# Performance work log

Measured on AMD Instinct MI355X. Metric: run time of the kernel, lower is better.

## Reference

```python
import jax, jax.numpy as jnp
import numpy as np

B, T, N, F = 32, 64, 128, 128
U, K1, K2 = 64, 64, 32
EPS = 1e-3  # keras BatchNormalization default epsilon
SLOPE = 0.01  # LeakyReLU negative_slope


def setup_inputs() -> dict:
    key = jax.random.key(0)
    ks = jax.random.split(key, 16)
    g = lambda k, sh, s=0.05: jax.random.normal(k, sh, dtype=jnp.float32) * s
    inp = {
        "x": jax.random.normal(ks[0], (B, T, F), dtype=jnp.float32),
        "a": jax.random.uniform(ks[1], (B, N, N), dtype=jnp.float32),
        # LSTM (keras gate order i, f, c, o)
        "lstm_k": g(ks[2], (F, 4 * U)),
        "lstm_r": g(ks[3], (U, 4 * U)),
        "lstm_b": jnp.zeros((4 * U,), jnp.float32),
        # BatchNorm params (inference form: gamma, beta, moving mean, moving var)
        "bnl_g": jnp.ones((U,), jnp.float32), "bnl_b": jnp.zeros((U,), jnp.float32),
        "bnl_m": jnp.zeros((U,), jnp.float32), "bnl_v": jnp.ones((U,), jnp.float32),
        "w1": g(ks[4], (U, K1)), "b1": jnp.zeros((K1,), jnp.float32),
        "bn1_g": jnp.ones((K1,), jnp.float32), "bn1_b": jnp.zeros((K1,), jnp.float32),
        "bn1_m": jnp.zeros((K1,), jnp.float32), "bn1_v": jnp.ones((K1,), jnp.float32),
        "w2": g(ks[5], (K1, K2)), "b2": jnp.zeros((K2,), jnp.float32),
        "bn2_g": jnp.ones((K2,), jnp.float32), "bn2_b": jnp.zeros((K2,), jnp.float32),
        "bn2_m": jnp.zeros((K2,), jnp.float32), "bn2_v": jnp.ones((K2,), jnp.float32),
        "d1_w": g(ks[6], (T * N * K2, 3), 0.01), "d1_b": jnp.zeros((3,), jnp.float32),
        "d2_w": g(ks[7], (3, N)), "d2_b": jnp.zeros((N,), jnp.float32),
    }
    return inp


def _bn(x, g, b, m, v):
    return (x - m) * (g * jax.lax.rsqrt(v + EPS)) + b


def _leaky(x):
    return jnp.where(x >= 0, x, SLOPE * x)


def _lstm(x, Wk, Wr, b):
    # x: [B, T, F] -> hs: [B, T, U]
    xz = jnp.einsum('btf,fg->btg', x, Wk) + b  # precompute input projections
    u = Wr.shape[0]
    h0 = jnp.zeros((x.shape[0], u), x.dtype)
    c0 = jnp.zeros((x.shape[0], u), x.dtype)

    def step(carry, zt):
        h, c = carry
        z = zt + h @ Wr
        i, f, g_, o = jnp.split(z, 4, axis=-1)
        i = jax.nn.sigmoid(i); f = jax.nn.sigmoid(f)
        g_ = jnp.tanh(g_); o = jax.nn.sigmoid(o)
        c = f * c + i * g_
        h = o * jnp.tanh(c)
        return (h, c), h

    _, hs = jax.lax.scan(step, (h0, c0), xz.transpose(1, 0, 2))
    return hs.transpose(1, 0, 2)


def reference(x, a, lstm_k, lstm_r, lstm_b, bnl_g, bnl_b, bnl_m, bnl_v,
              w1, b1, bn1_g, bn1_b, bn1_m, bn1_v,
              w2, b2, bn2_g, bn2_b, bn2_m, bn2_v,
              d1_w, d1_b, d2_w, d2_b):
    h = _lstm(x, lstm_k, lstm_r, lstm_b)              # [B, T, U]
    h = _bn(h, bnl_g, bnl_b, bnl_m, bnl_v)            # inference BN; dropout is identity
    # tile each timestep's LSTM output over the N nodes, then GCN1
    support1 = jnp.einsum('btu,uk->btk', h, w1)       # [B, T, K1] (identical across nodes)
    sup1 = jnp.broadcast_to(support1[:, :, None, :], (h.shape[0], h.shape[1], N, w1.shape[1]))
    g1 = jnp.einsum('bij,btjk->btik', a, sup1) + b1   # adjacency matmul
    g1 = _leaky(g1)
    g1 = _bn(g1, bn1_g, bn1_b, bn1_m, bn1_v)
    # GCN2
    sup2 = jnp.einsum('btnk,km->btnm', g1, w2)
    g2 = jnp.einsum('bij,btjm->btim', a, sup2) + b2
    g2 = _leaky(g2)
    g2 = _bn(g2, bn2_g, bn2_b, bn2_m, bn2_v)          # [B, T, N, K2]
    flat = g2.reshape(g2.shape[0], -1)                # [B, T*N*K2]
    d1 = jax.nn.relu(flat @ d1_w + d1_b)              # [B, 3]
    return d1 @ d2_w + d2_b                           # [B, N]
```

## Files before the change

kernel.cpp:

```cpp
#include <hip/hip_runtime.h>

#define BB 32
#define TT 64
#define NN 128
#define FF 128
#define UU 64
#define K1 64
#define K2 32
#define G4 256
#define EPSV 1e-3f
#define SLOPE 0.01f

#define ALD 136
#define SLD 136
#define WLD 72

typedef __attribute__((ext_vector_type(8))) short short8;
typedef __attribute__((ext_vector_type(4))) float f32x4;
typedef __attribute__((ext_vector_type(2))) __fp16 half2v;

__device__ __forceinline__ float sigmoidf_(float x) {
  return __builtin_amdgcn_rcpf(1.f + __expf(-x));
}
__device__ __forceinline__ float tanhf_(float x) {
  return 1.f - 2.f * __builtin_amdgcn_rcpf(__expf(2.f * x) + 1.f);
}
__device__ __forceinline__ float leaky_(float x) { return x >= 0.f ? x : SLOPE * x; }
__device__ __forceinline__ unsigned short f2bf(float x) {
  union { float f; unsigned u; } v; v.f = x;
  unsigned r = v.u + 0x7fff + ((v.u >> 16) & 1);
  return (unsigned short)(r >> 16);
}

__global__ __launch_bounds__(256) void k_xzp(const float* __restrict__ x,
                                             const float* __restrict__ wk,
                                             const float* __restrict__ bias,
                                             const float* __restrict__ wr,
                                             const float* __restrict__ w1,
                                             float* __restrict__ xz,
                                             unsigned* __restrict__ wrp,
                                             unsigned* __restrict__ w1p) {
  int tid = threadIdx.x;
  if (blockIdx.x < 256) {
    __shared__ float xs[8][FF];
    int row0 = blockIdx.x * 8;
    for (int i = tid; i < 8 * FF; i += 256) xs[i >> 7][i & 127] = x[(size_t)row0 * FF + i];
    __syncthreads();
    int g = tid;
    float acc[8];
    float bg = bias[g];
#pragma unroll
    for (int r = 0; r < 8; ++r) acc[r] = bg;
    for (int f = 0; f < FF; ++f) {
      float w = wk[f * G4 + g];
#pragma unroll
      for (int r = 0; r < 8; ++r) acc[r] += xs[r][f] * w;
    }
#pragma unroll
    for (int r = 0; r < 8; ++r) xz[(size_t)(row0 + r) * G4 + g] = acc[r];
  } else if (blockIdx.x == 256) {
    for (int idx = tid; idx < 4 * 32 * UU; idx += 256) {
      int p = idx & 31;
      int gate = (idx >> 5) & 3;
      int u = idx >> 7;
      int col = gate * UU + u;
      union { __fp16 h[2]; unsigned u; } pk;
      pk.h[0] = (__fp16)wr[(2 * p) * G4 + col];
      pk.h[1] = (__fp16)wr[(2 * p + 1) * G4 + col];
      wrp[idx] = pk.u;
    }
  } else {
    for (int idx = tid; idx < 32 * K1; idx += 256) {
      int p = idx & 31, k = idx >> 5;
      union { __fp16 h[2]; unsigned u; } pk;
      pk.h[0] = (__fp16)w1[(2 * p) * K1 + k];
      pk.h[1] = (__fp16)w1[(2 * p + 1) * K1 + k];
      w1p[idx] = pk.u;
    }
  }
}

__global__ __launch_bounds__(256, 1) void k_mega(
    const float* __restrict__ xz, const unsigned* __restrict__ wrp,
    const unsigned* __restrict__ w1p,
    const float* __restrict__ bnl_g, const float* __restrict__ bnl_b,
    const float* __restrict__ bnl_m, const float* __restrict__ bnl_v,
    const float* __restrict__ a, const float* __restrict__ w2,
    const float* __restrict__ d1w,
    float* __restrict__ s1out, float* __restrict__ rsum,
    unsigned short* __restrict__ apad, unsigned short* __restrict__ w2t,
    float4* __restrict__ d1r) {
  __shared__ __align__(16) char smem[76032];
  int tid = threadIdx.x;
  int blk = blockIdx.x;

  if (blk < 32) {
    float* xz_lds = (float*)smem;
    __fp16* hp = (__fp16*)(smem + 65536);
    float* zex = (float*)(smem + 73728);
    __fp16* h16 = (__fp16*)(smem + 75776);
    int wave = tid >> 6, lane = tid & 63;
    int role = wave & 1;
    int b = blk;

    {
      const float4* src = (const float4*)(xz + (size_t)b * TT * G4);
      float4* dst = (float4*)xz_lds;
#pragma unroll
      for (int k = 0; k < 16; ++k) dst[tid + k * 256] = src[tid + k * 256];
    }
    unsigned wv0[32], wv1[32];
    if (wave < 2) {
      const uint4* wp = (const uint4*)(wrp + (size_t)lane * 128 + role * 64);
#pragma unroll
      for (int k = 0; k < 8; ++k) {
        uint4 v = wp[k];
        wv0[4 * k + 0] = v.x; wv0[4 * k + 1] = v.y; wv0[4 * k + 2] = v.z; wv0[4 * k + 3] = v.w;
      }
#pragma unroll
      for (int k = 0; k < 8; ++k) {
        uint4 v = wp[8 + k];
        wv1[4 * k + 0] = v.x; wv1[4 * k + 1] = v.y; wv1[4 * k + 2] = v.z; wv1[4 * k + 3] = v.w;
      }
      h16[wave * UU + lane] = (__fp16)0.f;
    }
    float bscale = bnl_g[lane] * rsqrtf(bnl_v[lane] + EPSV);
    float boff = bnl_b[lane] - bnl_m[lane] * bscale;
    float c = 0.f;
    __syncthreads();

    for (int t = 0; t < TT; ++t) {
      int par = t & 1;
      float z0, z1;
      if (wave < 2) {
        __builtin_amdgcn_sched_barrier(0);
        unsigned hw[32];
        const uint4* hq = (const uint4*)(h16 + wave * UU);
#pragma unroll
        for (int k = 0; k < 8; ++k) {
          uint4 v = hq[k];
          hw[4 * k + 0] = v.x; hw[4 * k + 1] = v.y; hw[4 * k + 2] = v.z; hw[4 * k + 3] = v.w;
        }
        z0 = xz_lds[t * G4 + role * 128 + lane];
        z1 = xz_lds[t * G4 + role * 128 + 64 + lane];
#pragma unroll
        for (int p = 0; p < 32; ++p) {
          half2v hh = __builtin_bit_cast(half2v, hw[p]);
          z0 = __builtin_amdgcn_fdot2(__builtin_bit_cast(half2v, wv0[p]), hh, z0, false);
          z1 = __builtin_amdgcn_fdot2(__builtin_bit_cast(half2v, wv1[p]), hh, z1, false);
        }
        zex[(par * 2 + role) * 128 + lane] = z0;
        zex[(par * 2 + role) * 128 + 64 + lane] = z1;
      }
      __syncthreads();
      if (wave < 2) {
        float pz0 = zex[(par * 2 + (role ^ 1)) * 128 + lane];
        float pz1 = zex[(par * 2 + (role ^ 1)) * 128 + 64 + lane];
        float zi = role ? pz0 : z0;
        float zf = role ? pz1 : z1;
        float zg = role ? z0 : pz0;
        float zo = role ? z1 : pz1;
        float i_ = sigmoidf_(zi), f_ = sigmoidf_(zf), g_ = tanhf_(zg), o_ = sigmoidf_(zo);
        c = f_ * c + i_ * g_;
        float h = o_ * tanhf_(c);
        h16[wave * UU + lane] = (__fp16)h;
        __builtin_amdgcn_sched_barrier(0);
        if (role == 0) hp[t * UU + lane] = (__fp16)(h * bscale + boff);
      }
    }
    __syncthreads();

    unsigned w1v[32];
    {
      const uint4* wp1 = (const uint4*)(w1p + (size_t)lane * 32);
#pragma unroll
      for (int k = 0; k < 8; ++k) {
        uint4 v = wp1[k];
        w1v[4 * k + 0] = v.x; w1v[4 * k + 1] = v.y; w1v[4 * k + 2] = v.z; w1v[4 * k + 3] = v.w;
      }
    }
    float* s1b = s1out + (size_t)b * TT * K1;
    for (int r = 0; r < 16; ++r) {
      int t = wave * 16 + r;
      unsigned hw2[32];
      const uint4* hq = (const uint4*)(hp + t * UU);
#pragma unroll
      for (int k = 0; k < 8; ++k) {
        uint4 v = hq[k];
        hw2[4 * k + 0] = v.x; hw2[4 * k + 1] = v.y; hw2[4 * k + 2] = v.z; hw2[4 * k + 3] = v.w;
      }
      float acc = 0.f;
#pragma unroll
      for (int p = 0; p < 32; ++p)
        acc = __builtin_amdgcn_fdot2(__builtin_bit_cast(half2v, w1v[p]),
                                     __builtin_bit_cast(half2v, hw2[p]), acc, false);
      s1b[t * K1 + lane] = acc;
    }
  } else if (blk < 64) {
    int b = blk - 32;
    int wave = tid >> 6, lane = tid & 63;
    const float* ab = a + (size_t)b * NN * NN;
    for (int r = 0; r < 32; ++r) {
      int row = wave * 32 + r;
      float2 v = *(const float2*)(ab + (size_t)row * NN + lane * 2);
      float s = v.x + v.y;
#pragma unroll
      for (int off = 32; off >= 1; off >>= 1) s += __shfl_down(s, off);
      if (lane == 0) rsum[b * NN + row] = s;
    }
    unsigned short* ap = apad + (size_t)b * NN * ALD;
    for (int idx = tid; idx < NN * NN; idx += 256) {
      int i = idx >> 7, j = idx & 127;
      ap[i * ALD + j] = f2bf(ab[idx]);
    }
  } else if (blk == 64) {
    for (int idx = tid; idx < K1 * K2; idx += 256) {
      int k = idx >> 5, m = idx & 31;
      w2t[m * WLD + k] = f2bf(w2[idx]);
    }
  } else {
    int t = blk - 65;
    float* dt = (float*)smem;
    const float* src = d1w + (size_t)t * NN * K2 * 3;
    for (int c32 = 0; c32 < 4; ++c32) {
      __syncthreads();
      for (int i = tid; i < 768; i += 256)
        ((float4*)dt)[i] = ((const float4*)(src + c32 * 3072))[i];
      __syncthreads();
#pragma unroll
      for (int q = 0; q < 3; ++q) {
        int item = q * 256 + tid;
        int l = item & 63;
        int gc = item >> 6;
        int g = gc / 3, cc = gc % 3;
        int it = g >> 1, mt = g & 1;
        int l15v = l & 15, l4v = l >> 4;
        int m = mt * 16 + l15v;
        int rowbase = it * 16 + l4v * 4;
        float4 v;
        v.x = dt[(rowbase + 0) * 96 + m * 3 + cc];
        v.y = dt[(rowbase + 1) * 96 + m * 3 + cc];
        v.z = dt[(rowbase + 2) * 96 + m * 3 + cc];
        v.w = dt[(rowbase + 3) * 96 + m * 3 + cc];
        d1r[(((size_t)t * 4 + g) * 3 + cc) * 256 + c32 * 64 + l] = v;
      }
    }
  }
}

__global__ __launch_bounds__(256) void k_gcn(
    const float* __restrict__ s1g, const float* __restrict__ rsum,
    const unsigned short* __restrict__ apad, const unsigned short* __restrict__ w2t,
    const float* __restrict__ b1,
    const float* __restrict__ bn1_g, const float* __restrict__ bn1_b,
    const float* __restrict__ bn1_m, const float* __restrict__ bn1_v,
    const float* __restrict__ b2,
    const float* __restrict__ bn2_g, const float* __restrict__ bn2_b,
    const float* __restrict__ bn2_m, const float* __restrict__ bn2_v,
    const float4* __restrict__ d1r, float* __restrict__ part) {
  __shared__ unsigned short s2_lds[K2 * SLD];
  __shared__ float s1l[2][K1];
  __shared__ float4 gp[K1];
  __shared__ float r_lds[NN];
  __shared__ float p2[3 * K2];
  __shared__ float red[12];

  int blk = blockIdx.x;
  int b = blk & 31, tg = blk >> 5;
  int t0 = tg * 2;
  int tid = threadIdx.x;
  int lane = tid & 63, wave = tid >> 6;
  int l15 = lane & 15, l4 = lane >> 4;

  const unsigned short* ab = apad + (size_t)b * NN * ALD;
  short8 afrag[4][2];
#pragma unroll
  for (int kt = 0; kt < 4; ++kt)
#pragma unroll
    for (int it = 0; it < 2; ++it) {
      int i = (wave * 2 + it) * 16 + l15;
      afrag[kt][it] = *((const short8*)&ab[i * ALD + kt * 32 + l4 * 8]);
    }
  short8 bw[2][2];
#pragma unroll
  for (int kt = 0; kt < 2; ++kt) {
    bw[kt][0] = *((const short8*)&w2t[(0 + l15) * WLD + kt * 32 + l4 * 8]);
    bw[kt][1] = *((const short8*)&w2t[(16 + l15) * WLD + kt * 32 + l4 * 8]);
  }

  if (tid < 128) ((float*)s1l)[tid] = s1g[((size_t)b * TT + t0) * K1 + tid];
  if (tid < K1) {
    float s = bn1_g[tid] * rsqrtf(bn1_v[tid] + EPSV);
    gp[tid] = make_float4(b1[tid], s, bn1_b[tid] - bn1_m[tid] * s, 0.f);
  }
  if (tid >= 64 && tid < 192) r_lds[tid - 64] = rsum[b * NN + (tid - 64)];
  if (tid >= 192 && tid < 192 + K2) {
    int m = tid - 192;
    float s = bn2_g[m] * rsqrtf(bn2_v[m] + EPSV);
    p2[m] = b2[m];
    p2[K2 + m] = s;
    p2[2 * K2 + m] = bn2_b[m] - bn2_m[m] * s;
  }
  __syncthreads();

  f32x4 z4 = {0.f, 0.f, 0.f, 0.f};
  float rj0 = r_lds[(wave * 2 + 0) * 16 + l15];
  float rj1 = r_lds[(wave * 2 + 1) * 16 + l15];

  float c0 = 0.f, c1 = 0.f, c2 = 0.f;

  for (int ti = 0; ti < 2; ++ti) {
    int t = t0 + ti;
    f32x4 a1[2][2];
    a1[0][0] = z4; a1[0][1] = z4; a1[1][0] = z4; a1[1][1] = z4;
#pragma unroll
    for (int kt = 0; kt < 2; ++kt) {
      float4 gpv[8];
      float s1v[8];
#pragma unroll
      for (int e = 0; e < 8; ++e) {
        gpv[e] = gp[kt * 32 + l4 * 8 + e];
        s1v[e] = s1l[ti][kt * 32 + l4 * 8 + e];
      }
#pragma unroll
      for (int jt = 0; jt < 2; ++jt) {
        float rj = jt ? rj1 : rj0;
        short8 af;
#pragma unroll
        for (int e = 0; e < 8; ++e) {
          float4 p = gpv[e];
          float v = leaky_(rj * s1v[e] + p.x) * p.y + p.z;
          af[e] = (short)f2bf(v);
        }
        a1[jt][0] = __builtin_amdgcn_mfma_f32_16x16x32_bf16(af, bw[kt][0], a1[jt][0], 0, 0, 0);
        a1[jt][1] = __builtin_amdgcn_mfma_f32_16x16x32_bf16(af, bw[kt][1], a1[jt][1], 0, 0, 0);
      }
    }
    __syncthreads();
#pragma unroll
    for (int jt = 0; jt < 2; ++jt) {
      int jbase = (wave * 2 + jt) * 16 + l4 * 4;
#pragma unroll
      for (int mt = 0; mt < 2; ++mt) {
        int m = mt * 16 + l15;
        unsigned lo = (unsigned)f2bf(a1[jt][mt][0]) | ((unsigned)f2bf(a1[jt][mt][1]) << 16);
        unsigned hi = (unsigned)f2bf(a1[jt][mt][2]) | ((unsigned)f2bf(a1[jt][mt][3]) << 16);
        uint2 val; val.x = lo; val.y = hi;
        *((uint2*)&s2_lds[m * SLD + jbase]) = val;
      }
    }
    __syncthreads();

    f32x4 acc[2][2];
    acc[0][0] = z4; acc[0][1] = z4; acc[1][0] = z4; acc[1][1] = z4;
#pragma unroll
    for (int kt = 0; kt < 4; ++kt) {
      short8 bfrag0 = *((const short8*)&s2_lds[(0 + l15) * SLD + kt * 32 + l4 * 8]);
      short8 bfrag1 = *((const short8*)&s2_lds[(16 + l15) * SLD + kt * 32 + l4 * 8]);
#pragma unroll
      for (int it = 0; it < 2; ++it) {
        acc[it][0] = __builtin_amdgcn_mfma_f32_16x16x32_bf16(afrag[kt][it], bfrag0, acc[it][0], 0, 0, 0);
        acc[it][1] = __builtin_amdgcn_mfma_f32_16x16x32_bf16(afrag[kt][it], bfrag1, acc[it][1], 0, 0, 0);
      }
    }
    float gv[2][2][4];
#pragma unroll
    for (int it = 0; it < 2; ++it)
#pragma unroll
      for (int mt = 0; mt < 2; ++mt) {
        int m = mt * 16 + l15;
        float bb = p2[m], bs = p2[K2 + m], bo = p2[2 * K2 + m];
#pragma unroll
        for (int r = 0; r < 4; ++r) gv[it][mt][r] = leaky_(acc[it][mt][r] + bb) * bs + bo;
      }
#pragma unroll
    for (int g = 0; g < 4; ++g) {
      int it = g >> 1, mt = g & 1;
      float4 v0 = d1r[(((size_t)t * 4 + g) * 3 + 0) * 256 + tid];
      float4 v1 = d1r[(((size_t)t * 4 + g) * 3 + 1) * 256 + tid];
      float4 v2 = d1r[(((size_t)t * 4 + g) * 3 + 2) * 256 + tid];
      c0 += gv[it][mt][0] * v0.x + gv[it][mt][1] * v0.y + gv[it][mt][2] * v0.z + gv[it][mt][3] * v0.w;
      c1 += gv[it][mt][0] * v1.x + gv[it][mt][1] * v1.y + gv[it][mt][2] * v1.z + gv[it][mt][3] * v1.w;
      c2 += gv[it][mt][0] * v2.x + gv[it][mt][1] * v2.y + gv[it][mt][2] * v2.z + gv[it][mt][3] * v2.w;
    }
  }

#pragma unroll
  for (int off = 32; off >= 1; off >>= 1) {
    c0 += __shfl_down(c0, off);
    c1 += __shfl_down(c1, off);
    c2 += __shfl_down(c2, off);
  }
  if (lane == 0) { red[wave * 3 + 0] = c0; red[wave * 3 + 1] = c1; red[wave * 3 + 2] = c2; }
  __syncthreads();
  if (tid == 0) {
    float s0 = 0.f, s1v = 0.f, s2v = 0.f;
    for (int w = 0; w < 4; ++w) { s0 += red[w * 3]; s1v += red[w * 3 + 1]; s2v += red[w * 3 + 2]; }
    part[((size_t)b * 32 + tg) * 3 + 0] = s0;
    part[((size_t)b * 32 + tg) * 3 + 1] = s1v;
    part[((size_t)b * 32 + tg) * 3 + 2] = s2v;
  }
}

__global__ __launch_bounds__(128) void k_out(const float* __restrict__ part,
                                             const float* __restrict__ d1b,
                                             const float* __restrict__ d2w,
                                             const float* __restrict__ d2b,
                                             float* __restrict__ out) {
  int b = blockIdx.x, n = threadIdx.x;
  float s[3] = {0.f, 0.f, 0.f};
  const float* p = part + (size_t)b * 32 * 3;
#pragma unroll
  for (int g = 0; g < 32; ++g) {
    s[0] += p[g * 3];
    s[1] += p[g * 3 + 1];
    s[2] += p[g * 3 + 2];
  }
  float o = d2b[n];
#pragma unroll
  for (int c = 0; c < 3; ++c) {
    float d = s[c] + d1b[c];
    d = d > 0.f ? d : 0.f;
    o += d * d2w[c * NN + n];
  }
  out[b * NN + n] = o;
}

extern "C" void kernel_launch(void* const* d_in, const int* in_sizes, int n_in,
                              void* d_out, int out_size, void* d_ws, size_t ws_size,
                              hipStream_t stream) {
  const float* x      = (const float*)d_in[0];
  const float* a      = (const float*)d_in[1];
  const float* lstm_k = (const float*)d_in[2];
  const float* lstm_r = (const float*)d_in[3];
  const float* lstm_b = (const float*)d_in[4];
  const float* bnl_g  = (const float*)d_in[5];
  const float* bnl_b  = (const float*)d_in[6];
  const float* bnl_m  = (const float*)d_in[7];
  const float* bnl_v  = (const float*)d_in[8];
  const float* w1     = (const float*)d_in[9];
  const float* b1     = (const float*)d_in[10];
  const float* bn1_g  = (const float*)d_in[11];
  const float* bn1_b  = (const float*)d_in[12];
  const float* bn1_m  = (const float*)d_in[13];
  const float* bn1_v  = (const float*)d_in[14];
  const float* w2     = (const float*)d_in[15];
  const float* b2     = (const float*)d_in[16];
  const float* bn2_g  = (const float*)d_in[17];
  const float* bn2_b  = (const float*)d_in[18];
  const float* bn2_m  = (const float*)d_in[19];
  const float* bn2_v  = (const float*)d_in[20];
  const float* d1_w   = (const float*)d_in[21];
  const float* d1_b   = (const float*)d_in[22];
  const float* d2_w   = (const float*)d_in[23];
  const float* d2_b   = (const float*)d_in[24];
  float* out = (float*)d_out;

  char* ws = (char*)d_ws;
  float* xz            = (float*)(ws + 0);
  float* s1            = (float*)(ws + 2097152);
  float* rsum          = (float*)(ws + 2621440);
  float* part          = (float*)(ws + 2637824);
  unsigned short* apad = (unsigned short*)(ws + 2662400);
  unsigned short* w2t  = (unsigned short*)(ws + 3776512);
  unsigned* wrp        = (unsigned*)(ws + 3781120);
  unsigned* w1p        = (unsigned*)(ws + 3813888);
  float4* d1r          = (float4*)(ws + 3822080);

  k_xzp<<<258, 256, 0, stream>>>(x, lstm_k, lstm_b, lstm_r, w1, xz, wrp, w1p);
  k_mega<<<129, 256, 0, stream>>>(xz, wrp, w1p, bnl_g, bnl_b, bnl_m, bnl_v,
                                  a, w2, d1_w, s1, rsum, apad, w2t, d1r);
  k_gcn<<<1024, 256, 0, stream>>>(s1, rsum, apad, w2t, b1, bn1_g, bn1_b, bn1_m, bn1_v,
                                  b2, bn2_g, bn2_b, bn2_m, bn2_v, d1r, part);
  k_out<<<BB, 128, 0, stream>>>(part, d1_b, d2_w, d2_b, out);
}
```

Measured before the change: 69.85 us.

## Run each LSTM batch in a single wave without per-step block barriers

Each wave computes all four gates for one batch element, holding the full recurrent weight slice in registers. This removes the per-timestep LDS gate exchange and __syncthreads between paired waves. Input projections are now prefetched one step ahead from global memory instead of being staged in LDS. Blocks are widened to 512 threads, packing 8 batches into each LSTM block, and the auxiliary block roles are re-indexed. The cost is doubled dot-product work per lane and higher register pressure, which risks spills.

```diff
diff --git a/kernel.cpp b/kernel.cpp
--- a/kernel.cpp
+++ b/kernel.cpp
@@ -80,7 +80,7 @@
   }
 }
 
-__global__ __launch_bounds__(256, 1) void k_mega(
+__global__ __launch_bounds__(512, 1) void k_mega(
     const float* __restrict__ xz, const unsigned* __restrict__ wrp,
     const unsigned* __restrict__ w1p,
     const float* __restrict__ bnl_g, const float* __restrict__ bnl_b,
@@ -90,85 +90,66 @@
     float* __restrict__ s1out, float* __restrict__ rsum,
     unsigned short* __restrict__ apad, unsigned short* __restrict__ w2t,
     float4* __restrict__ d1r) {
-  __shared__ __align__(16) char smem[76032];
+  __shared__ __align__(16) char smem[86016];
   int tid = threadIdx.x;
   int blk = blockIdx.x;
 
-  if (blk < 32) {
-    float* xz_lds = (float*)smem;
-    __fp16* hp = (__fp16*)(smem + 65536);
-    float* zex = (float*)(smem + 73728);
-    __fp16* h16 = (__fp16*)(smem + 75776);
+  if (blk < 4) {
     int wave = tid >> 6, lane = tid & 63;
-    int role = wave & 1;
-    int b = blk;
-
+    int b = blk * 8 + wave;
+    __fp16* hpw = (__fp16*)smem + (size_t)wave * TT * UU;
+    __fp16* h16w = (__fp16*)(smem + 65536) + wave * UU;
+
+    unsigned wv[4][32];
     {
-      const float4* src = (const float4*)(xz + (size_t)b * TT * G4);
-      float4* dst = (float4*)xz_lds;
-#pragma unroll
-      for (int k = 0; k < 16; ++k) dst[tid + k * 256] = src[tid + k * 256];
-    }
-    unsigned wv0[32], wv1[32];
-    if (wave < 2) {
-      const uint4* wp = (const uint4*)(wrp + (size_t)lane * 128 + role * 64);
-#pragma unroll
-      for (int k = 0; k < 8; ++k) {
+      const uint4* wp = (const uint4*)(wrp + (size_t)lane * 128);
+#pragma unroll
+      for (int k = 0; k < 32; ++k) {
         uint4 v = wp[k];
-        wv0[4 * k + 0] = v.x; wv0[4 * k + 1] = v.y; wv0[4 * k + 2] = v.z; wv0[4 * k + 3] = v.w;
-      }
-#pragma unroll
-      for (int k = 0; k < 8; ++k) {
-        uint4 v = wp[8 + k];
-        wv1[4 * k + 0] = v.x; wv1[4 * k + 1] = v.y; wv1[4 * k + 2] = v.z; wv1[4 * k + 3] = v.w;
-      }
-      h16[wave * UU + lane] = (__fp16)0.f;
+        int gate = k >> 3, p0 = (k & 7) * 4;
+        wv[gate][p0 + 0] = v.x; wv[gate][p0 + 1] = v.y;
+        wv[gate][p0 + 2] = v.z; wv[gate][p0 + 3] = v.w;
+      }
     }
     float bscale = bnl_g[lane] * rsqrtf(bnl_v[lane] + EPSV);
     float boff = bnl_b[lane] - bnl_m[lane] * bscale;
+    h16w[lane] = (__fp16)0.f;
     float c = 0.f;
-    __syncthreads();
+
+    const float* xzb = xz + (size_t)b * TT * G4;
+    float cz0 = xzb[lane], cz1 = xzb[64 + lane], cz2 = xzb[128 + lane], cz3 = xzb[192 + lane];
 
     for (int t = 0; t < TT; ++t) {
-      int par = t & 1;
-      float z0, z1;
-      if (wave < 2) {
-        __builtin_amdgcn_sched_barrier(0);
-        unsigned hw[32];
-        const uint4* hq = (const uint4*)(h16 + wave * UU);
+      int tn = (t + 1 < TT) ? t + 1 : t;
+      const float* nb = xzb + tn * G4;
+      float nz0 = nb[lane], nz1 = nb[64 + lane], nz2 = nb[128 + lane], nz3 = nb[192 + lane];
+      __builtin_amdgcn_sched_barrier(0);
+      unsigned hw[32];
+      {
+        const uint4* hq = (const uint4*)h16w;
 #pragma unroll
         for (int k = 0; k < 8; ++k) {
           uint4 v = hq[k];
           hw[4 * k + 0] = v.x; hw[4 * k + 1] = v.y; hw[4 * k + 2] = v.z; hw[4 * k + 3] = v.w;
         }
-        z0 = xz_lds[t * G4 + role * 128 + lane];
-        z1 = xz_lds[t * G4 + role * 128 + 64 + lane];
-#pragma unroll
-        for (int p = 0; p < 32; ++p) {
-          half2v hh = __builtin_bit_cast(half2v, hw[p]);
-          z0 = __builtin_amdgcn_fdot2(__builtin_bit_cast(half2v, wv0[p]), hh, z0, false);
-          z1 = __builtin_amdgcn_fdot2(__builtin_bit_cast(half2v, wv1[p]), hh, z1, false);
-        }
-        zex[(par * 2 + role) * 128 + lane] = z0;
-        zex[(par * 2 + role) * 128 + 64 + lane] = z1;
-      }
-      __syncthreads();
-      if (wave < 2) {
-        float pz0 = zex[(par * 2 + (role ^ 1)) * 128 + lane];
-        float pz1 = zex[(par * 2 + (role ^ 1)) * 128 + 64 + lane];
-        float zi = role ? pz0 : z0;
-        float zf = role ? pz1 : z1;
-        float zg = role ? z0 : pz0;
-        float zo = role ? z1 : pz1;
-        float i_ = sigmoidf_(zi), f_ = sigmoidf_(zf), g_ = tanhf_(zg), o_ = sigmoidf_(zo);
-        c = f_ * c + i_ * g_;
-        float h = o_ * tanhf_(c);
-        h16[wave * UU + lane] = (__fp16)h;
-        __builtin_amdgcn_sched_barrier(0);
-        if (role == 0) hp[t * UU + lane] = (__fp16)(h * bscale + boff);
-      }
-    }
-    __syncthreads();
+      }
+      float z0 = cz0, z1 = cz1, z2 = cz2, z3 = cz3;
+#pragma unroll
+      for (int p = 0; p < 32; ++p) {
+        half2v hh = __builtin_bit_cast(half2v, hw[p]);
+        z0 = __builtin_amdgcn_fdot2(__builtin_bit_cast(half2v, wv[0][p]), hh, z0, false);
+        z1 = __builtin_amdgcn_fdot2(__builtin_bit_cast(half2v, wv[1][p]), hh, z1, false);
+        z2 = __builtin_amdgcn_fdot2(__builtin_bit_cast(half2v, wv[2][p]), hh, z2, false);
+        z3 = __builtin_amdgcn_fdot2(__builtin_bit_cast(half2v, wv[3][p]), hh, z3, false);
+      }
+      float i_ = sigmoidf_(z0), f_ = sigmoidf_(z1), g_ = tanhf_(z2), o_ = sigmoidf_(z3);
+      c = f_ * c + i_ * g_;
+      float h = o_ * tanhf_(c);
+      h16w[lane] = (__fp16)h;
+      __builtin_amdgcn_sched_barrier(0);
+      hpw[t * UU + lane] = (__fp16)(h * bscale + boff);
+      cz0 = nz0; cz1 = nz1; cz2 = nz2; cz3 = nz3;
+    }
 
     unsigned w1v[32];
     {
@@ -180,14 +161,15 @@
       }
     }
     float* s1b = s1out + (size_t)b * TT * K1;
-    for (int r = 0; r < 16; ++r) {
-      int t = wave * 16 + r;
+    for (int t = 0; t < TT; ++t) {
       unsigned hw2[32];
-      const uint4* hq = (const uint4*)(hp + t * UU);
-#pragma unroll
-      for (int k = 0; k < 8; ++k) {
-        uint4 v = hq[k];
-        hw2[4 * k + 0] = v.x; hw2[4 * k + 1] = v.y; hw2[4 * k + 2] = v.z; hw2[4 * k + 3] = v.w;
+      {
+        const uint4* hq = (const uint4*)(hpw + t * UU);
+#pragma unroll
+        for (int k = 0; k < 8; ++k) {
+          uint4 v = hq[k];
+          hw2[4 * k + 0] = v.x; hw2[4 * k + 1] = v.y; hw2[4 * k + 2] = v.z; hw2[4 * k + 3] = v.w;
+        }
       }
       float acc = 0.f;
 #pragma unroll
@@ -196,12 +178,12 @@
                                      __builtin_bit_cast(half2v, hw2[p]), acc, false);
       s1b[t * K1 + lane] = acc;
     }
-  } else if (blk < 64) {
-    int b = blk - 32;
+  } else if (blk < 36) {
+    int b = blk - 4;
     int wave = tid >> 6, lane = tid & 63;
     const float* ab = a + (size_t)b * NN * NN;
-    for (int r = 0; r < 32; ++r) {
-      int row = wave * 32 + r;
+    for (int r = 0; r < 16; ++r) {
+      int row = wave * 16 + r;
       float2 v = *(const float2*)(ab + (size_t)row * NN + lane * 2);
       float s = v.x + v.y;
 #pragma unroll
@@ -209,40 +191,42 @@
       if (lane == 0) rsum[b * NN + row] = s;
     }
     unsigned short* ap = apad + (size_t)b * NN * ALD;
-    for (int idx = tid; idx < NN * NN; idx += 256) {
+    for (int idx = tid; idx < NN * NN; idx += 512) {
       int i = idx >> 7, j = idx & 127;
       ap[i * ALD + j] = f2bf(ab[idx]);
     }
-  } else if (blk == 64) {
-    for (int idx = tid; idx < K1 * K2; idx += 256) {
+  } else if (blk == 36) {
+    for (int idx = tid; idx < K1 * K2; idx += 512) {
       int k = idx >> 5, m = idx & 31;
       w2t[m * WLD + k] = f2bf(w2[idx]);
     }
   } else {
-    int t = blk - 65;
+    int t = blk - 37;
     float* dt = (float*)smem;
     const float* src = d1w + (size_t)t * NN * K2 * 3;
     for (int c32 = 0; c32 < 4; ++c32) {
       __syncthreads();
-      for (int i = tid; i < 768; i += 256)
+      for (int i = tid; i < 768; i += 512)
         ((float4*)dt)[i] = ((const float4*)(src + c32 * 3072))[i];
       __syncthreads();
 #pragma unroll
-      for (int q = 0; q < 3; ++q) {
-        int item = q * 256 + tid;
-        int l = item & 63;
-        int gc = item >> 6;
-        int g = gc / 3, cc = gc % 3;
-        int it = g >> 1, mt = g & 1;
-        int l15v = l & 15, l4v = l >> 4;
-        int m = mt * 16 + l15v;
-        int rowbase = it * 16 + l4v * 4;
-        float4 v;
-        v.x = dt[(rowbase + 0) * 96 + m * 3 + cc];
-        v.y = dt[(rowbase + 1) * 96 + m * 3 + cc];
-        v.z = dt[(rowbase + 2) * 96 + m * 3 + cc];
-        v.w = dt[(rowbase + 3) * 96 + m * 3 + cc];
-        d1r[(((size_t)t * 4 + g) * 3 + cc) * 256 + c32 * 64 + l] = v;
+      for (int q = 0; q < 2; ++q) {
+        int item = q * 512 + tid;
+        if (item < 768) {
+          int l = item & 63;
+          int gc = item >> 6;
+          int g = gc / 3, cc = gc % 3;
+          int it = g >> 1, mt = g & 1;
+          int l15v = l & 15, l4v = l >> 4;
+          int m = mt * 16 + l15v;
+          int rowbase = it * 16 + l4v * 4;
+          float4 v;
+          v.x = dt[(rowbase + 0) * 96 + m * 3 + cc];
+          v.y = dt[(rowbase + 1) * 96 + m * 3 + cc];
+          v.z = dt[(rowbase + 2) * 96 + m * 3 + cc];
+          v.w = dt[(rowbase + 3) * 96 + m * 3 + cc];
+          d1r[(((size_t)t * 4 + g) * 3 + cc) * 256 + c32 * 64 + l] = v;
+        }
       }
     }
   }
@@ -468,7 +452,7 @@
   float4* d1r          = (float4*)(ws + 3822080);
 
   k_xzp<<<258, 256, 0, stream>>>(x, lstm_k, lstm_b, lstm_r, w1, xz, wrp, w1p);
-  k_mega<<<129, 256, 0, stream>>>(xz, wrp, w1p, bnl_g, bnl_b, bnl_m, bnl_v,
+  k_mega<<<101, 512, 0, stream>>>(xz, wrp, w1p, bnl_g, bnl_b, bnl_m, bnl_v,
                                   a, w2, d1_w, s1, rsum, apad, w2t, d1r);
   k_gcn<<<1024, 256, 0, stream>>>(s1, rsum, apad, w2t, b1, bn1_g, bn1_b, bn1_m, bn1_v,
                                   b2, bn2_g, bn2_b, bn2_m, bn2_v, d1r, part);
```

Measured after the change: 98.28 us. +40.7%, slower.
